# Performance work log

Measured on AMD Instinct MI355X. Metric: run time of the kernel, lower is better.

## Reference

```python
import jax, jax.numpy as jnp
import numpy as np

N, C, H, W = 4, 128, 64, 64


def setup_inputs() -> dict:
    key = jax.random.key(0)
    ks = jax.random.split(key, 4)
    s = 1.0 / np.sqrt(C).astype(np.float32)  # conv2d default-init scale
    return {
        "x": jax.random.normal(ks[0], (N, C, H, W), dtype=jnp.float32),
        "Wq": jax.random.normal(ks[1], (C, C), dtype=jnp.float32) * s,
        "bq": jnp.zeros((C,), dtype=jnp.float32),
        "Wk": jax.random.normal(ks[2], (C, C), dtype=jnp.float32) * s,
        "bk": jnp.zeros((C,), dtype=jnp.float32),
        "Wv": jax.random.normal(ks[3], (C, C), dtype=jnp.float32) * s,
        "bv": jnp.zeros((C,), dtype=jnp.float32),
    }


def reference(x, Wq, bq, Wk, bk, Wv, bv):
    n, c, h, w = x.shape
    xf = x.reshape(n, c, h * w)  # [N, C, L], L = H*W
    # 1x1 convs == per-pixel channel mixing
    q = jnp.einsum('oc,ncl->nol', Wq, xf) + bq[:, None]
    k = jnp.einsum('oc,ncl->nol', Wk, xf) + bk[:, None]
    v = jnp.einsum('oc,ncl->nol', Wv, xf) + bv[:, None]
    # scores[l, m] = sum_c k[c,l] * q[c,m]  (matmul(k^T, q))
    scale = jnp.asarray(1.0 / np.sqrt(c), x.dtype)
    scores = jnp.einsum('ncl,ncm->nlm', k, q) * scale  # [N, L, L]
    temp = jax.nn.softmax(scores, axis=-1)
    attn = jnp.einsum('ncl,nlm->ncm', v, temp)  # [N, C, L]
    return x + attn.reshape(n, c, h, w)
```

## Files before the change

### kernel.cpp

```cpp
#include <hip/hip_runtime.h>
#include <hip/hip_bf16.h>
#include <stdint.h>

#define NB 4
#define CH 128
#define LL 4096

typedef __attribute__((ext_vector_type(8))) short short8;
typedef __attribute__((ext_vector_type(4))) short short4b;
typedef __attribute__((ext_vector_type(4))) float floatx4;
typedef __attribute__((ext_vector_type(16))) float floatx16;


static __device__ __forceinline__ short f2bf(float f) {
    uint32_t u = __float_as_uint(f);
    u += 0x7fffu + ((u >> 16) & 1u);
    return (short)(u >> 16);
}
static __device__ __forceinline__ float bf2f(short s) {
    return __uint_as_float(((uint32_t)(uint16_t)s) << 16);
}

__global__ __launch_bounds__(256) void wprep_kernel(
    const float* __restrict__ Wq, const float* __restrict__ Wk,
    const float* __restrict__ Wv, short* __restrict__ Wf)
{
    const int g = blockIdx.x * 256 + threadIdx.x;
    const int mat = g >> 14;
    const int rem = g & 16383;
    const int o   = rem >> 7;
    const int c   = rem & 127;
    const float* W = (mat == 0) ? Wq : (mat == 1) ? Wk : Wv;
    float v = W[o * CH + c];
    if (mat == 1) v *= 0.08838834764831845f;
    Wf[(size_t)mat * 16384 + (o >> 4) * 2048 + (c >> 5) * 512
       + ((c >> 3) & 3) * 128 + (o & 15) * 8 + (c & 7)] = f2bf(v);
}

__global__ __launch_bounds__(256) void proj_kernel(
    const float* __restrict__ x, const short* __restrict__ Wf,
    const float* __restrict__ bq, const float* __restrict__ bk,
    const float* __restrict__ bv,
    short* __restrict__ Qf, short* __restrict__ Kf, short* __restrict__ Vp)
{
    const int i    = blockIdx.x;
    const int n    = (i >> 1) & 3;
    const int lt   = ((i >> 3) << 1) | (i & 1);
    const int l0   = lt << 5;
    const int tid  = threadIdx.x;
    const int wave = tid >> 6;
    const int lane = tid & 63;
    const int quad = lane >> 4;
    const int mc   = lane & 15;

    __shared__ short Xb[32][136];

    {
        const int sl = tid & 31;
        const int cg = tid >> 5;
        const float* xp = x + ((size_t)n * CH + cg * 16) * LL + l0 + sl;
        short8 buf;
        #pragma unroll
        for (int i2 = 0; i2 < 16; ++i2) {
            buf[i2 & 7] = f2bf(xp[(size_t)i2 * LL]);
            if ((i2 & 7) == 7)
                *(short8*)(void*)&Xb[sl][cg * 16 + (i2 & 8)] = buf;
        }
    }
    __syncthreads();

    const int lt2 = wave >> 1;
    const int oh  = wave & 1;
    const int gt  = lt * 2 + lt2;

    short8 xf[4];
    #pragma unroll
    for (int s = 0; s < 4; ++s)
        xf[s] = *(const short8*)(const void*)&Xb[lt2 * 16 + mc][32 * s + quad * 8];

    const size_t obase = ((size_t)n * 256 + gt) * 2048;
    const float scale = 0.08838834764831845f;

    #pragma unroll
    for (int mat = 0; mat < 3; ++mat) {
        const short* Wm = Wf + (size_t)mat * 16384;
        const float* bb = (mat == 0) ? bq : (mat == 1) ? bk : bv;
        const float bscale = (mat == 1) ? scale : 1.0f;
        #pragma unroll
        for (int ot = oh * 4; ot < oh * 4 + 4; ++ot) {
            floatx4 acc = {0.f, 0.f, 0.f, 0.f};
            #pragma unroll
            for (int s = 0; s < 4; ++s)
                acc = __builtin_amdgcn_mfma_f32_16x16x32_bf16(
                    *(const short8*)(const void*)(Wm + ot * 2048 + s * 512 + lane * 8),
                    xf[s], acc, 0, 0, 0);
            const int c0 = ot * 16 + 4 * quad;
            if (mat < 2) {
                short4b pv;
                #pragma unroll
                for (int r = 0; r < 4; ++r)
                    pv[r] = f2bf(acc[r] + bb[c0 + r] * bscale);
                short* dst = ((mat == 0) ? Qf : Kf) + obase
                           + (c0 >> 5) * 512 + ((c0 >> 3) & 3) * 128
                           + mc * 8 + (c0 & 7);
                *(short4b*)(void*)dst = pv;
            } else {
                #pragma unroll
                for (int r = 0; r < 4; ++r)
                    Vp[obase + (c0 + r) * 16 + mc] = f2bf(acc[r] + bb[c0 + r]);
            }
        }
    }
}

__global__ __launch_bounds__(512, 4) void rowsum_kernel(
    const short* __restrict__ Qf, const short* __restrict__ Kf,
    float* __restrict__ Dv)
{
    const int i    = blockIdx.x;
    const int n    = (i >> 1) & 3;
    const int tp   = ((i >> 3) << 1) | (i & 1);
    const int tid  = threadIdx.x;
    const int wave = tid >> 6;
    const int lane = tid & 63;
    const int quad = lane >> 4;
    const int mc   = lane & 15;

    __shared__ float Db[8][32];

    const short* Kb = Kf + ((size_t)n * 256 + tp * 2) * 2048 + lane * 8;
    short8 kf[2][4];
    #pragma unroll
    for (int t = 0; t < 2; ++t)
        #pragma unroll
        for (int s = 0; s < 4; ++s)
            kf[t][s] = *(const short8*)(const void*)(Kb + t * 2048 + s * 512);

    const short* Qn = Qf + (size_t)n * 524288 + (size_t)wave * 32 * 2048 + lane * 8;
    float rs[2][4] = {{0.f, 0.f, 0.f, 0.f}, {0.f, 0.f, 0.f, 0.f}};

    short8 qA[4], qB[4];
    #pragma unroll
    for (int s = 0; s < 4; ++s)
        qA[s] = *(const short8*)(const void*)(Qn + s * 512);

    auto qstep = [&](const short8 (&q)[4]) {
        floatx4 a0 = {0.f, 0.f, 0.f, 0.f};
        floatx4 a1 = {0.f, 0.f, 0.f, 0.f};
        #pragma unroll
        for (int s = 0; s < 4; ++s) {
            a0 = __builtin_amdgcn_mfma_f32_16x16x32_bf16(kf[0][s], q[s], a0, 0, 0, 0);
            a1 = __builtin_amdgcn_mfma_f32_16x16x32_bf16(kf[1][s], q[s], a1, 0, 0, 0);
        }
        #pragma unroll
        for (int r = 0; r < 4; ++r) {
            rs[0][r] += __expf(a0[r]);
            rs[1][r] += __expf(a1[r]);
        }
    };

    for (int it = 0; it < 32; it += 2) {
        #pragma unroll
        for (int s = 0; s < 4; ++s)
            qB[s] = *(const short8*)(const void*)(
                Qn + (size_t)((it + 1) & 31) * 2048 + s * 512);
        qstep(qA);
        #pragma unroll
        for (int s = 0; s < 4; ++s)
            qA[s] = *(const short8*)(const void*)(
                Qn + (size_t)((it + 2) & 31) * 2048 + s * 512);
        qstep(qB);
    }

    #pragma unroll
    for (int t = 0; t < 2; ++t)
        #pragma unroll
        for (int r = 0; r < 4; ++r) {
            float v = rs[t][r];
            v += __shfl_xor(v, 1);
            v += __shfl_xor(v, 2);
            v += __shfl_xor(v, 4);
            v += __shfl_xor(v, 8);
            if (mc == 0) Db[wave][t * 16 + quad * 4 + r] = v;
        }
    __syncthreads();
    if (tid < 32) {
        float s = 0.f;
        #pragma unroll
        for (int m = 0; m < 8; ++m) s += Db[m][tid];
        Dv[(size_t)n * 4096 + tp * 32 + tid] = 1.0f / s;
    }
}

__global__ __launch_bounds__(512, 4) void attn_out_kernel(
    const short* __restrict__ Qf, const short* __restrict__ Kf,
    const short* __restrict__ Vp, const float* __restrict__ Dv,
    float* __restrict__ Po)
{
    const int i    = blockIdx.x;
    const int n    = (i >> 1) & 3;
    const int j    = ((i >> 3) << 1) | (i & 1);
    const int lh   = j >> 6;
    const int mb   = j & 63;
    const int m0   = mb << 6;
    const int tid  = threadIdx.x;
    const int wave = tid >> 6;
    const int lane = tid & 63;
    const int quad = lane >> 4;
    const int mc   = lane & 15;
    const int l32  = lane & 31;
    const int h    = lane >> 5;
    const int ct   = wave & 3;
    const int mh   = wave >> 2;

    __shared__ short P[2][64][264];

    const short* Qn  = Qf + (size_t)n * 524288;
    const short* Kn  = Kf + (size_t)n * 524288;
    const short* Vpn = Vp + (size_t)n * 524288;
    const float* Dn  = Dv + (size_t)n * 4096;
    const int tile0  = lh * 128;

    floatx16 acc;
    #pragma unroll
    for (int r = 0; r < 16; ++r) acc[r] = 0.f;

    for (int t = 0; t < 8; ++t) {
        const int p = t & 1;

        {
            const int tb = tile0 + t * 16 + 2 * wave;
            short8 kfr[2][4];
            #pragma unroll
            for (int jj = 0; jj < 2; ++jj)
                #pragma unroll
                for (int s = 0; s < 4; ++s)
                    kfr[jj][s] = *(const short8*)(const void*)(
                        Kn + (size_t)(tb + jj) * 2048 + s * 512 + lane * 8);
            floatx4 dr[2];
            #pragma unroll
            for (int jj = 0; jj < 2; ++jj)
                dr[jj] = *(const floatx4*)(const void*)(
                    Dn + (tb + jj) * 16 + quad * 4);

            #pragma unroll
            for (int mst = 0; mst < 4; ++mst) {
                short8 qt[4];
                #pragma unroll
                for (int s = 0; s < 4; ++s)
                    qt[s] = *(const short8*)(const void*)(
                        Qn + (size_t)((m0 >> 4) + mst) * 2048 + s * 512 + lane * 8);
                floatx4 sa0 = {0.f, 0.f, 0.f, 0.f};
                floatx4 sa1 = {0.f, 0.f, 0.f, 0.f};
                #pragma unroll
                for (int s = 0; s < 4; ++s) {
                    sa0 = __builtin_amdgcn_mfma_f32_16x16x32_bf16(kfr[0][s], qt[s], sa0, 0, 0, 0);
                    sa1 = __builtin_amdgcn_mfma_f32_16x16x32_bf16(kfr[1][s], qt[s], sa1, 0, 0, 0);
                }
                short4b pv0, pv1;
                #pragma unroll
                for (int r = 0; r < 4; ++r) {
                    pv0[r] = f2bf(__expf(sa0[r]) * dr[0][r]);
                    pv1[r] = f2bf(__expf(sa1[r]) * dr[1][r]);
                }
                *(short4b*)(void*)&P[p][16 * mst + mc][32 * wave + quad * 4] = pv0;
                *(short4b*)(void*)&P[p][16 * mst + mc][32 * wave + 16 + quad * 4] = pv1;
            }
        }
        __syncthreads();

        #pragma unroll
        for (int kc = 0; kc < 16; ++kc) {
            const short8 vf = *(const short8*)(const void*)(
                Vpn + (size_t)(tile0 + t * 16 + kc) * 2048
                    + (32 * ct + l32) * 16 + 8 * h);
            const short8 pf = *(const short8*)(const void*)&P[p][32 * mh + l32][16 * kc + 8 * h];
            acc = __builtin_amdgcn_mfma_f32_32x32x16_bf16(vf, pf, acc, 0, 0, 0);
        }
    }

    float* Pon = Po + (size_t)(lh * 4 + n) * 524288;
    #pragma unroll
    for (int r = 0; r < 16; ++r) {
        const int c = 32 * ct + (r & 3) + 8 * (r >> 2) + 4 * h;
        const int m = m0 + 32 * mh + l32;
        Pon[(size_t)c * LL + m] = acc[r];
    }
}

__global__ __launch_bounds__(256) void combine_kernel(
    const float* __restrict__ x, const float* __restrict__ Po,
    float* __restrict__ out)
{
    const size_t k = (size_t)blockIdx.x * 256 + threadIdx.x;
    const floatx4 a = *(const floatx4*)(const void*)(x + 4 * k);
    const floatx4 b = *(const floatx4*)(const void*)(Po + 4 * k);
    const floatx4 c = *(const floatx4*)(const void*)(Po + 2097152 + 4 * k);
    floatx4 o;
    #pragma unroll
    for (int r = 0; r < 4; ++r) o[r] = a[r] + b[r] + c[r];
    *(floatx4*)(void*)(out + 4 * k) = o;
}

extern "C" void kernel_launch(void* const* d_in, const int* in_sizes, int n_in,
                              void* d_out, int out_size, void* d_ws, size_t ws_size,
                              hipStream_t stream) {
    (void)in_sizes; (void)n_in; (void)out_size; (void)ws_size;
    const float* x  = (const float*)d_in[0];
    const float* Wq = (const float*)d_in[1];
    const float* bq = (const float*)d_in[2];
    const float* Wk = (const float*)d_in[3];
    const float* bk = (const float*)d_in[4];
    const float* Wv = (const float*)d_in[5];
    const float* bv = (const float*)d_in[6];
    float* out = (float*)d_out;

    char* ws = (char*)d_ws;
    short* Qf = (short*)(ws);
    short* Kf = (short*)(ws + 4194304);
    short* Vp = (short*)(ws + 8388608);
    float* Dv = (float*)(ws + 12582912);
    short* Wf = (short*)(ws + 16777216);
    float* Po = (float*)(ws + 16908288);

    wprep_kernel<<<192, 256, 0, stream>>>(Wq, Wk, Wv, Wf);
    proj_kernel<<<512, 256, 0, stream>>>(x, Wf, bq, bk, bv, Qf, Kf, Vp);
    rowsum_kernel<<<512, 512, 0, stream>>>(Qf, Kf, Dv);
    attn_out_kernel<<<512, 512, 0, stream>>>(Qf, Kf, Vp, Dv, Po);
    combine_kernel<<<2048, 256, 0, stream>>>(x, Po, out);
}
```

Before: 157.8 us.

## Split attn accumulator, prefetch V before barrier, widen rowsum blocks to 1024 threads

In the attention-output kernel, the single MFMA accumulator is split into two interleaved chains, and the first two V fragments are loaded before the barrier. This shortens the MFMA dependency chain and hides global load latency, and the P tile padding also changes from 264 to 260. The rowsum kernel is reorganised into 256 blocks of 1024 threads, each covering 64 key rows, so each Q stream load serves twice as many keys. The cost is more accumulator registers, and the new padding may bring LDS bank conflicts.

```diff
diff --git a/kernel.cpp b/kernel.cpp
--- a/kernel.cpp
+++ b/kernel.cpp
@@ -113,22 +113,24 @@
     }
 }
 
-__global__ __launch_bounds__(512, 4) void rowsum_kernel(
+__global__ __launch_bounds__(1024) void rowsum_kernel(
     const short* __restrict__ Qf, const short* __restrict__ Kf,
     float* __restrict__ Dv)
 {
     const int i    = blockIdx.x;
     const int n    = (i >> 1) & 3;
-    const int tp   = ((i >> 3) << 1) | (i & 1);
+    const int tq   = ((i >> 3) << 1) | (i & 1);
     const int tid  = threadIdx.x;
     const int wave = tid >> 6;
     const int lane = tid & 63;
     const int quad = lane >> 4;
     const int mc   = lane & 15;
-
-    __shared__ float Db[8][32];
-
-    const short* Kb = Kf + ((size_t)n * 256 + tp * 2) * 2048 + lane * 8;
+    const int mw   = wave & 7;
+    const int th   = wave >> 3;
+
+    __shared__ float Db[16][32];
+
+    const short* Kb = Kf + ((size_t)n * 256 + tq * 4 + th * 2) * 2048 + lane * 8;
     short8 kf[2][4];
     #pragma unroll
     for (int t = 0; t < 2; ++t)
@@ -136,7 +138,7 @@
         for (int s = 0; s < 4; ++s)
             kf[t][s] = *(const short8*)(const void*)(Kb + t * 2048 + s * 512);
 
-    const short* Qn = Qf + (size_t)n * 524288 + (size_t)wave * 32 * 2048 + lane * 8;
+    const short* Qn = Qf + (size_t)n * 524288 + (size_t)mw * 32 * 2048 + lane * 8;
     float rs[2][4] = {{0.f, 0.f, 0.f, 0.f}, {0.f, 0.f, 0.f, 0.f}};
 
     short8 qA[4], qB[4];
@@ -184,11 +186,12 @@
             if (mc == 0) Db[wave][t * 16 + quad * 4 + r] = v;
         }
     __syncthreads();
-    if (tid < 32) {
+    if (tid < 64) {
+        const int lh = tid >> 5, lr = tid & 31;
         float s = 0.f;
         #pragma unroll
-        for (int m = 0; m < 8; ++m) s += Db[m][tid];
-        Dv[(size_t)n * 4096 + tp * 32 + tid] = 1.0f / s;
+        for (int m = 0; m < 8; ++m) s += Db[lh * 8 + m][lr];
+        Dv[(size_t)n * 4096 + tq * 64 + tid] = 1.0f / s;
     }
 }
 
@@ -213,7 +216,7 @@
     const int ct   = wave & 3;
     const int mh   = wave >> 2;
 
-    __shared__ short P[2][64][264];
+    __shared__ short P[2][64][260];
 
     const short* Qn  = Qf + (size_t)n * 524288;
     const short* Kn  = Kf + (size_t)n * 524288;
@@ -221,15 +224,18 @@
     const float* Dn  = Dv + (size_t)n * 4096;
     const int tile0  = lh * 128;
 
-    floatx16 acc;
-    #pragma unroll
-    for (int r = 0; r < 16; ++r) acc[r] = 0.f;
+    const size_t vcol = (size_t)(32 * ct + l32) * 16 + 8 * h;
+
+    floatx16 acc0, acc1;
+    #pragma unroll
+    for (int r = 0; r < 16; ++r) { acc0[r] = 0.f; acc1[r] = 0.f; }
 
     for (int t = 0; t < 8; ++t) {
-        const int p = t & 1;
+        const int p   = t & 1;
+        const int tb0 = tile0 + t * 16;
 
         {
-            const int tb = tile0 + t * 16 + 2 * wave;
+            const int tb = tb0 + 2 * wave;
             short8 kfr[2][4];
             #pragma unroll
             for (int jj = 0; jj < 2; ++jj)
@@ -267,15 +273,30 @@
                 *(short4b*)(void*)&P[p][16 * mst + mc][32 * wave + 16 + quad * 4] = pv1;
             }
         }
+
+        const short8 vp0 = *(const short8*)(const void*)(
+            Vpn + (size_t)(tb0 + 0) * 2048 + vcol);
+        const short8 vp1 = *(const short8*)(const void*)(
+            Vpn + (size_t)(tb0 + 1) * 2048 + vcol);
+
         __syncthreads();
 
-        #pragma unroll
-        for (int kc = 0; kc < 16; ++kc) {
-            const short8 vf = *(const short8*)(const void*)(
-                Vpn + (size_t)(tile0 + t * 16 + kc) * 2048
-                    + (32 * ct + l32) * 16 + 8 * h);
-            const short8 pf = *(const short8*)(const void*)&P[p][32 * mh + l32][16 * kc + 8 * h];
-            acc = __builtin_amdgcn_mfma_f32_32x32x16_bf16(vf, pf, acc, 0, 0, 0);
+        {
+            const short8 pf0 = *(const short8*)(const void*)&P[p][32 * mh + l32][8 * h];
+            acc0 = __builtin_amdgcn_mfma_f32_32x32x16_bf16(vp0, pf0, acc0, 0, 0, 0);
+            const short8 pf1 = *(const short8*)(const void*)&P[p][32 * mh + l32][16 + 8 * h];
+            acc1 = __builtin_amdgcn_mfma_f32_32x32x16_bf16(vp1, pf1, acc1, 0, 0, 0);
+        }
+        #pragma unroll
+        for (int kc = 2; kc < 16; kc += 2) {
+            const short8 vfa = *(const short8*)(const void*)(
+                Vpn + (size_t)(tb0 + kc) * 2048 + vcol);
+            const short8 pfa = *(const short8*)(const void*)&P[p][32 * mh + l32][16 * kc + 8 * h];
+            acc0 = __builtin_amdgcn_mfma_f32_32x32x16_bf16(vfa, pfa, acc0, 0, 0, 0);
+            const short8 vfb = *(const short8*)(const void*)(
+                Vpn + (size_t)(tb0 + kc + 1) * 2048 + vcol);
+            const short8 pfb = *(const short8*)(const void*)&P[p][32 * mh + l32][16 * (kc + 1) + 8 * h];
+            acc1 = __builtin_amdgcn_mfma_f32_32x32x16_bf16(vfb, pfb, acc1, 0, 0, 0);
         }
     }
 
@@ -284,7 +305,7 @@
     for (int r = 0; r < 16; ++r) {
         const int c = 32 * ct + (r & 3) + 8 * (r >> 2) + 4 * h;
         const int m = m0 + 32 * mh + l32;
-        Pon[(size_t)c * LL + m] = acc[r];
+        Pon[(size_t)c * LL + m] = acc0[r] + acc1[r];
     }
 }
 
@@ -325,7 +346,7 @@
 
     wprep_kernel<<<192, 256, 0, stream>>>(Wq, Wk, Wv, Wf);
     proj_kernel<<<512, 256, 0, stream>>>(x, Wf, bq, bk, bv, Qf, Kf, Vp);
-    rowsum_kernel<<<512, 512, 0, stream>>>(Qf, Kf, Dv);
+    rowsum_kernel<<<256, 1024, 0, stream>>>(Qf, Kf, Dv);
     attn_out_kernel<<<512, 512, 0, stream>>>(Qf, Kf, Vp, Dv, Po);
     combine_kernel<<<2048, 256, 0, stream>>>(x, Po, out);
 }
```

New measurement: 205.0 us. 29.9% more time.
